# Kernel optimization log

Measured on AMD Instinct MI355X. Metric: run time of the kernel, lower is better.

The kernel has to match this reference:

```python
import jax, jax.numpy as jnp
import numpy as np

N_OBJ, N_REL = 5000, 20000
HID, POOL, N_RELCLS, N_OBJCLS = 512, 4096, 51, 151


def setup_inputs() -> dict:
    key = jax.random.key(0)
    ks = jax.random.split(key, 8)
    s = lambda fi, fo: (2.0 / (fi + fo)) ** 0.5  # xavier-ish scale
    return {
        'edge_ctx': jax.random.normal(ks[0], (N_OBJ, HID), jnp.float32),
        'union_features': jax.random.normal(ks[1], (N_REL, POOL), jnp.float32),
        'W_pe': jax.random.normal(ks[2], (2 * HID, HID), jnp.float32) * (10.0 * (1.0 / HID) ** 0.5),
        'b_pe': jnp.zeros((2 * HID,), jnp.float32),
        'W_pc': jax.random.normal(ks[3], (POOL, 2 * HID), jnp.float32) * s(2 * HID, POOL),
        'b_pc': jnp.zeros((POOL,), jnp.float32),
        'W_cc': jax.random.normal(ks[4], (N_RELCLS, POOL), jnp.float32) * s(POOL, N_RELCLS),
        'b_cc': jnp.zeros((N_RELCLS,), jnp.float32),
        'freq_emb': jax.random.normal(ks[5], (N_OBJCLS * N_OBJCLS, N_RELCLS), jnp.float32) * 0.1,
        'obj_preds': jax.random.randint(ks[6], (N_OBJ,), 0, N_OBJCLS, jnp.int64 if jax.config.jax_enable_x64 else jnp.int32),
        'pair_idx': jax.random.randint(ks[7], (N_REL, 2), 0, N_OBJ, jnp.int64 if jax.config.jax_enable_x64 else jnp.int32),
    }


def reference(edge_ctx, union_features, W_pe, b_pe, W_pc, b_pc, W_cc, b_cc,
              freq_emb, obj_preds, pair_idx):
    # post_emb -> relu -> split into head/tail halves ([N,2,HID] view)
    edge_rep = jax.nn.relu(edge_ctx @ W_pe.T + b_pe)          # [N, 2*HID]
    head_rep, tail_rep = edge_rep[:, :HID], edge_rep[:, HID:]

    hi, ti = pair_idx[:, 0], pair_idx[:, 1]
    prod = jnp.concatenate([head_rep[hi], tail_rep[ti]], axis=-1)  # [R, 2*HID]
    prod_rep = prod @ W_pc.T + b_pc                               # [R, POOL]

    ctx_dists = (prod_rep * union_features) @ W_cc.T + b_cc      # [R, 51]

    # frequency bias: embedding lookup at head_cls * num_obj_cls + tail_cls
    pair_lbl = obj_preds[hi] * N_OBJCLS + obj_preds[ti]
    frq_dists = freq_emb[pair_lbl]                               # [R, 51]
    # dropout p=0.3 is identity in eval mode
    return ctx_dists + frq_dists
```

## Files before the change

### kernel.cpp

```cpp
#include <hip/hip_runtime.h>

typedef unsigned short u16;
typedef unsigned int u32;
typedef __attribute__((ext_vector_type(4))) float f32x4;
typedef __attribute__((ext_vector_type(8))) __bf16 bf16x8;
typedef __attribute__((ext_vector_type(8))) u16 u16x8;

__device__ __forceinline__ u16 f2bf(float x) {
  u32 u = __float_as_uint(x);
  u32 r = (u + 0x7FFFu + ((u >> 16) & 1u)) >> 16;
  return (u16)r;
}

__device__ __forceinline__ float bf2f(u16 b) {
  return __uint_as_float((u32)b << 16);
}

__device__ __forceinline__ void gl16(const void* g, void* l) {
  auto* gp = (__attribute__((address_space(1))) u32*)(g);
  auto* lp = (__attribute__((address_space(3))) u32*)(l);
  __builtin_amdgcn_global_load_lds(gp, lp, 16, 0, 0);
}

__device__ __forceinline__ f32x4 mfma16(bf16x8 a, bf16x8 b, f32x4 c) {
  return __builtin_amdgcn_mfma_f32_16x16x32_bf16(a, b, c, 0, 0, 0);
}

__device__ __forceinline__ u16x8 cvt8(const float* p) {
  float4 a = *(const float4*)p, b = *(const float4*)(p + 4);
  u16x8 v;
  v[0] = f2bf(a.x); v[1] = f2bf(a.y); v[2] = f2bf(a.z); v[3] = f2bf(a.w);
  v[4] = f2bf(b.x); v[5] = f2bf(b.y); v[6] = f2bf(b.z); v[7] = f2bf(b.w);
  return v;
}

__global__ void k_prep(const float* __restrict__ ec, const float* __restrict__ wpe,
                       const float* __restrict__ wpc, const float* __restrict__ wcc,
                       u16* __restrict__ ecb, u16* __restrict__ wpeb,
                       u16* __restrict__ wpcb, u16* __restrict__ wccb) {
  int i = blockIdx.x * 256 + threadIdx.x;
  if (i < 320000) {
    *(u16x8*)(ecb + (long)i * 8) = cvt8(ec + (long)i * 8);
  } else if (i < 385536) {
    int j = i - 320000;
    *(u16x8*)(wpeb + (long)j * 8) = cvt8(wpe + (long)j * 8);
  } else if (i < 909824) {
    int j = i - 385536;
    *(u16x8*)(wpcb + (long)j * 8) = cvt8(wpc + (long)j * 8);
  } else if (i < 942592) {
    int j = i - 909824;
    long base = (long)j * 8;
    int row = (int)(base >> 12);
    int col = (int)(base & 4095);
    u16x8 v;
    if (row < 51) {
      v = cvt8(wcc + (long)row * 4096 + col);
    } else {
#pragma unroll
      for (int k = 0; k < 8; ++k) v[k] = 0;
    }
    *(u16x8*)(wccb + base) = v;
  }
}

__device__ __forceinline__ void cstep(const char* sA, const char* sB,
                                      const int (&aOff)[4], const int (&bOff)[4],
                                      f32x4 (&acc)[4][4]) {
  bf16x8 af[4], bv[4];
#pragma unroll
  for (int mi = 0; mi < 4; ++mi) af[mi] = *(const bf16x8*)(sA + aOff[mi]);
#pragma unroll
  for (int ni = 0; ni < 4; ++ni) bv[ni] = *(const bf16x8*)(sB + bOff[ni]);
  __builtin_amdgcn_s_setprio(1);
#pragma unroll
  for (int mi = 0; mi < 4; ++mi)
#pragma unroll
    for (int ni = 0; ni < 4; ++ni)
      acc[mi][ni] = mfma16(af[mi], bv[ni], acc[mi][ni]);
  __builtin_amdgcn_s_setprio(0);
}

__global__ __launch_bounds__(256, 2) void k_gemm1(const u16* __restrict__ A, const u16* __restrict__ B,
                                                  const float* __restrict__ bias, u16* __restrict__ outp) {
  __shared__ char lds[65536];
  int bx = blockIdx.x;
  int rb = bx >> 3, nb = bx & 7;
  int rowBase = rb * 128, nBase = nb * 128;
  int t = threadIdx.x, lane = t & 63, wid = t >> 6;
  int wr = wid >> 1, wc = wid & 1, lm = lane & 15, lg = lane >> 4;
  int ar0 = t >> 2, ar1 = 64 + ar0, c4 = t & 3;
  int sw0 = (c4 * 16) ^ (((ar0 >> 1) & 3) << 4);
  int sw1 = (c4 * 16) ^ (((ar1 >> 1) & 3) << 4);
  const char* aS0 = (const char*)(A + (long)min(rowBase + ar0, 4999) * 512) + sw0;
  const char* aS1 = (const char*)(A + (long)min(rowBase + ar1, 4999) * 512) + sw1;
  const char* bS0 = (const char*)(B + (long)(nBase + ar0) * 512) + sw0;
  const char* bS1 = (const char*)(B + (long)(nBase + ar1) * 512) + sw1;
  int t16 = t * 16;
  int aOff[4], bOff[4];
#pragma unroll
  for (int mi = 0; mi < 4; ++mi) { int r = wr * 64 + mi * 16 + lm; aOff[mi] = r * 64 + ((lg * 16) ^ (((r >> 1) & 3) << 4)); }
#pragma unroll
  for (int ni = 0; ni < 4; ++ni) { int r = wc * 64 + ni * 16 + lm; bOff[ni] = r * 64 + ((lg * 16) ^ (((r >> 1) & 3) << 4)); }
  f32x4 acc[4][4] = {};

#define STAGE_G(k, sb) do { \
    gl16(aS0 + (k) * 2, (sb) + t16); gl16(aS1 + (k) * 2, (sb) + 4096 + t16); \
    gl16(bS0 + (k) * 2, (sb) + 8192 + t16); gl16(bS1 + (k) * 2, (sb) + 12288 + t16); \
  } while (0)

  STAGE_G(0, lds);
  STAGE_G(32, lds + 16384);
  STAGE_G(64, lds + 32768);

  int cur = 0, stg = 3;
  for (int kt = 0; kt < 16; ++kt) {
    if (kt < 13) {
      char* sb = lds + stg * 16384;
      STAGE_G((kt + 3) * 32, sb);
    }
    if (kt < 13)       asm volatile("s_waitcnt vmcnt(12)" ::: "memory");
    else if (kt == 13) asm volatile("s_waitcnt vmcnt(8)" ::: "memory");
    else if (kt == 14) asm volatile("s_waitcnt vmcnt(4)" ::: "memory");
    else               asm volatile("s_waitcnt vmcnt(0)" ::: "memory");
    __builtin_amdgcn_s_barrier();
    char* cb = lds + cur * 16384;
    cstep(cb, cb + 8192, aOff, bOff, acc);
    __builtin_amdgcn_s_barrier();
    cur = (cur == 3) ? 0 : cur + 1;
    stg = (stg == 3) ? 0 : stg + 1;
  }
#undef STAGE_G

#pragma unroll
  for (int mi = 0; mi < 4; ++mi)
#pragma unroll
    for (int ni = 0; ni < 4; ++ni) {
      int n = nBase + wc * 64 + ni * 16 + lm;
      float bvv = bias[n];
#pragma unroll
      for (int rg = 0; rg < 4; ++rg) {
        int r = rowBase + wr * 64 + mi * 16 + lg * 4 + rg;
        if (r < 5000) {
          float v = acc[mi][ni][rg] + bvv;
          v = v > 0.f ? v : 0.f;
          outp[(long)r * 1024 + n] = f2bf(v);
        }
      }
    }
}

__global__ __launch_bounds__(256, 2) void k_gemm2(const u16* __restrict__ erep, const u16* __restrict__ wpc,
                                                  const float* __restrict__ bpc, u16* __restrict__ Hout,
                                                  u16* __restrict__ Tout) {
  __shared__ char lds[65536];
  int bx = blockIdx.x;
  int h = (bx >= 1280) ? 1 : 0;
  int rr = bx - h * 1280;
  int rb = rr >> 5, nb = rr & 31;
  int rowBase = rb * 128, nBase = nb * 128;
  u16* outp = h ? Tout : Hout;
  int t = threadIdx.x, lane = t & 63, wid = t >> 6;
  int wr = wid >> 1, wc = wid & 1, lm = lane & 15, lg = lane >> 4;
  int ar0 = t >> 2, ar1 = 64 + ar0, c4 = t & 3;
  int sw0 = (c4 * 16) ^ (((ar0 >> 1) & 3) << 4);
  int sw1 = (c4 * 16) ^ (((ar1 >> 1) & 3) << 4);
  const char* aS0 = (const char*)(erep + (long)min(rowBase + ar0, 4999) * 1024 + h * 512) + sw0;
  const char* aS1 = (const char*)(erep + (long)min(rowBase + ar1, 4999) * 1024 + h * 512) + sw1;
  const char* bS0 = (const char*)(wpc + (long)(nBase + ar0) * 1024 + h * 512) + sw0;
  const char* bS1 = (const char*)(wpc + (long)(nBase + ar1) * 1024 + h * 512) + sw1;
  int t16 = t * 16;
  int aOff[4], bOff[4];
#pragma unroll
  for (int mi = 0; mi < 4; ++mi) { int r = wr * 64 + mi * 16 + lm; aOff[mi] = r * 64 + ((lg * 16) ^ (((r >> 1) & 3) << 4)); }
#pragma unroll
  for (int ni = 0; ni < 4; ++ni) { int r = wc * 64 + ni * 16 + lm; bOff[ni] = r * 64 + ((lg * 16) ^ (((r >> 1) & 3) << 4)); }
  f32x4 acc[4][4] = {};

#define STAGE_G2(k, sb) do { \
    gl16(aS0 + (k) * 2, (sb) + t16); gl16(aS1 + (k) * 2, (sb) + 4096 + t16); \
    gl16(bS0 + (k) * 2, (sb) + 8192 + t16); gl16(bS1 + (k) * 2, (sb) + 12288 + t16); \
  } while (0)

  STAGE_G2(0, lds);
  STAGE_G2(32, lds + 16384);
  STAGE_G2(64, lds + 32768);

  int cur = 0, stg = 3;
  for (int kt = 0; kt < 16; ++kt) {
    if (kt < 13) {
      char* sb = lds + stg * 16384;
      STAGE_G2((kt + 3) * 32, sb);
    }
    if (kt < 13)       asm volatile("s_waitcnt vmcnt(12)" ::: "memory");
    else if (kt == 13) asm volatile("s_waitcnt vmcnt(8)" ::: "memory");
    else if (kt == 14) asm volatile("s_waitcnt vmcnt(4)" ::: "memory");
    else               asm volatile("s_waitcnt vmcnt(0)" ::: "memory");
    __builtin_amdgcn_s_barrier();
    char* cb = lds + cur * 16384;
    cstep(cb, cb + 8192, aOff, bOff, acc);
    __builtin_amdgcn_s_barrier();
    cur = (cur == 3) ? 0 : cur + 1;
    stg = (stg == 3) ? 0 : stg + 1;
  }
#undef STAGE_G2

#pragma unroll
  for (int mi = 0; mi < 4; ++mi)
#pragma unroll
    for (int ni = 0; ni < 4; ++ni) {
      int n = nBase + wc * 64 + ni * 16 + lm;
      float bvv = h ? 0.f : bpc[n];
#pragma unroll
      for (int rg = 0; rg < 4; ++rg) {
        int r = rowBase + wr * 64 + mi * 16 + lg * 4 + rg;
        if (r < 5000) {
          float v = acc[mi][ni][rg] + bvv;
          outp[(long)r * 4096 + n] = f2bf(v);
        }
      }
    }
}

__global__ __launch_bounds__(256) void k_final(
    const u16* __restrict__ H, const u16* __restrict__ T,
    const u16* __restrict__ wcc,
    const float* __restrict__ un,
    const int* __restrict__ pidx,
    float* __restrict__ partial) {
  __shared__ char sU[2][16384];
  int bx = blockIdx.x;
  int rb = bx >> 3, ps = bx & 7;
  int rowBase = rb * 64;
  int t = threadIdx.x, lane = t & 63, wid = t >> 6;
  int lm = lane & 15, lg = lane >> 4;
  int r16 = t >> 4, c16 = t & 15;

  u32 hoff[4], toff[4], uoff[4];
#pragma unroll
  for (int p = 0; p < 4; ++p) {
    int rG = min(rowBase + p * 16 + r16, 19999);
    hoff[p] = (u32)pidx[2 * rG] * 8192u + (u32)c16 * 16u;
    toff[p] = (u32)pidx[2 * rG + 1] * 8192u + (u32)c16 * 16u;
    uoff[p] = (u32)rG * 16384u + (u32)c16 * 32u;
  }
  const char* Hc = (const char*)H;
  const char* Tc = (const char*)T;
  const char* Uc = (const char*)un;
  int pc0 = ps * 512;

  u16x8 h8[4], t8[4];
  float4 u0[4], u1[4];

#define ISSUE(pcB) do { \
    _Pragma("unroll") \
    for (int p = 0; p < 4; ++p) { \
      h8[p] = *(const u16x8*)(Hc + hoff[p] + (u32)(pcB) * 2u); \
      t8[p] = *(const u16x8*)(Tc + toff[p] + (u32)(pcB) * 2u); \
      u0[p] = *(const float4*)(Uc + uoff[p] + (u32)(pcB) * 4u); \
      u1[p] = *(const float4*)(Uc + uoff[p] + (u32)(pcB) * 4u + 16u); \
    } \
  } while (0)

  f32x4 outAcc[4] = {};

  ISSUE(pc0);

  for (int chk = 0; chk < 4; ++chk) {
    int pcBase = pc0 + chk * 128;
    asm volatile("s_waitcnt vmcnt(0)" ::: "memory");
    char* sUb = sU[chk & 1];
#pragma unroll
    for (int p = 0; p < 4; ++p) {
      int r = p * 16 + r16;
      float uu[8];
      *(float4*)(uu) = u0[p];
      *(float4*)(uu + 4) = u1[p];
      bf16x8 pv;
#pragma unroll
      for (int j = 0; j < 8; ++j)
        pv[j] = (__bf16)((bf2f(h8[p][j]) + bf2f(t8[p][j])) * uu[j]);
      *(bf16x8*)(sUb + r * 256 + ((c16 * 16) ^ ((r & 7) << 4))) = pv;
    }
    bf16x8 bW[4][4];
#pragma unroll
    for (int kb = 0; kb < 4; ++kb)
#pragma unroll
      for (int ni = 0; ni < 4; ++ni)
        bW[kb][ni] = *(const bf16x8*)(wcc + (long)(ni * 16 + lm) * 4096 + pcBase + kb * 32 + lg * 8);
    if (chk < 3) ISSUE(pcBase + 128);
    asm volatile("s_waitcnt lgkmcnt(0)" ::: "memory");
    __builtin_amdgcn_s_barrier();

#pragma unroll
    for (int kb = 0; kb < 4; ++kb) {
      int r = wid * 16 + lm;
      bf16x8 aU = *(const bf16x8*)(sUb + r * 256 + ((kb * 64 + lg * 16) ^ ((r & 7) << 4)));
      __builtin_amdgcn_s_setprio(1);
#pragma unroll
      for (int ni = 0; ni < 4; ++ni)
        outAcc[ni] = mfma16(aU, bW[kb][ni], outAcc[ni]);
      __builtin_amdgcn_s_setprio(0);
    }
  }
#undef ISSUE

#pragma unroll
  for (int rg = 0; rg < 4; ++rg) {
    int r = wid * 16 + lg * 4 + rg;
    int rG = rowBase + r;
    if (rG < 20000) {
      long base = ((long)ps * 20000 + rG) * 64;
#pragma unroll
      for (int ni = 0; ni < 4; ++ni) {
        int c = ni * 16 + lm;
        if (c < 51) partial[base + c] = outAcc[ni][rg];
      }
    }
  }
}

__global__ void k_red(const float* __restrict__ partial, const float* __restrict__ bcc,
                      const float* __restrict__ freq, const int* __restrict__ preds,
                      const int* __restrict__ pidx, float* __restrict__ outp) {
  int idx = blockIdx.x * 256 + threadIdx.x;
  if (idx >= 20000 * 64) return;
  int row = idx >> 6, c = idx & 63;
  if (c >= 51) return;
  float s = 0.f;
#pragma unroll
  for (int i = 0; i < 8; ++i) s += partial[((long)i * 20000 + row) * 64 + c];
  int lbl = preds[pidx[2 * row]] * 151 + preds[pidx[2 * row + 1]];
  outp[(long)row * 51 + c] = s + bcc[c] + freq[(long)lbl * 51 + c];
}

extern "C" void kernel_launch(void* const* d_in, const int* in_sizes, int n_in,
                              void* d_out, int out_size, void* d_ws, size_t ws_size,
                              hipStream_t stream) {
  const float* edge_ctx = (const float*)d_in[0];
  const float* unionf   = (const float*)d_in[1];
  const float* W_pe     = (const float*)d_in[2];
  const float* b_pe     = (const float*)d_in[3];
  const float* W_pc     = (const float*)d_in[4];
  const float* b_pc     = (const float*)d_in[5];
  const float* W_cc     = (const float*)d_in[6];
  const float* b_cc     = (const float*)d_in[7];
  const float* freq     = (const float*)d_in[8];
  const int*   preds    = (const int*)d_in[9];
  const int*   pidx     = (const int*)d_in[10];
  float* out = (float*)d_out;
  char* ws = (char*)d_ws;

  u16* Hb    = (u16*)(ws + 0);
  u16* Tb    = (u16*)(ws + 40960000);
  u16* erep  = (u16*)(ws + 81920000);
  u16* wpcb  = (u16*)(ws + 92160000);
  u16* wccb  = (u16*)(ws + 100548608);
  u16* ecb   = (u16*)(ws + 101072896);
  u16* wpeb  = (u16*)(ws + 106192896);
  float* par = (float*)(ws + 107241472);

  k_prep<<<3682, 256, 0, stream>>>(edge_ctx, W_pe, W_pc, W_cc, ecb, wpeb, wpcb, wccb);
  k_gemm1<<<320, 256, 0, stream>>>(ecb, wpeb, b_pe, erep);
  k_gemm2<<<2560, 256, 0, stream>>>(erep, wpcb, b_pc, Hb, Tb);
  k_final<<<2504, 256, 0, stream>>>(Hb, Tb, wccb, unionf, pidx, par);
  k_red<<<5000, 256, 0, stream>>>(par, b_cc, freq, preds, pidx, out);
}
```

Before: 263.4 us.

## Split fused gather-multiply-GEMV into elementwise kernel plus pipelined GEMM

The fused final kernel, which gathered head/tail rows, multiplied them by union features and ran the MFMA reduction against W_cc, becomes two kernels. A grid-stride elementwise kernel writes the bf16 product matrix to workspace. A new GEMM then streams that product and W_cc through a four-stage LDS pipeline using direct global-to-LDS loads, with 128-row tiles and an 8-way K split. This aims to separate the latency-bound gather from the MFMA loop so each can be scheduled well, but it adds an extra round trip of a roughly 160 MB intermediate through memory.

```diff
diff --git a/kernel.cpp b/kernel.cpp
--- a/kernel.cpp
+++ b/kernel.cpp
@@ -221,102 +221,108 @@
     }
 }
 
-__global__ __launch_bounds__(256) void k_final(
-    const u16* __restrict__ H, const u16* __restrict__ T,
-    const u16* __restrict__ wcc,
-    const float* __restrict__ un,
-    const int* __restrict__ pidx,
-    float* __restrict__ partial) {
-  __shared__ char sU[2][16384];
+__global__ void k_mul(const u16* __restrict__ H, const u16* __restrict__ T,
+                      const float* __restrict__ un, const int* __restrict__ pidx,
+                      u16* __restrict__ P) {
+  long stride = (long)gridDim.x * 256;
+  for (long g = (long)blockIdx.x * 256 + threadIdx.x; g < 10240000; g += stride) {
+    int row = (int)(g >> 9);
+    int c8 = ((int)g & 511) * 8;
+    int hi = pidx[2 * row], ti = pidx[2 * row + 1];
+    u16x8 h8 = *(const u16x8*)(H + (long)hi * 4096 + c8);
+    u16x8 t8 = *(const u16x8*)(T + (long)ti * 4096 + c8);
+    const float* up = un + (long)row * 4096 + c8;
+    float4 u0 = *(const float4*)up, u1 = *(const float4*)(up + 4);
+    float uu[8];
+    *(float4*)(uu) = u0;
+    *(float4*)(uu + 4) = u1;
+    bf16x8 pv;
+#pragma unroll
+    for (int j = 0; j < 8; ++j)
+      pv[j] = (__bf16)((bf2f(h8[j]) + bf2f(t8[j])) * uu[j]);
+    *(bf16x8*)(P + g * 8) = pv;
+  }
+}
+
+__global__ __launch_bounds__(256, 2) void k_gemm3(const u16* __restrict__ P, const u16* __restrict__ wcc,
+                                                  float* __restrict__ partial) {
+  __shared__ char lds[49152];
   int bx = blockIdx.x;
-  int rb = bx >> 3, ps = bx & 7;
-  int rowBase = rb * 64;
+  int rb = bx >> 3, ks = bx & 7;
+  int rowBase = rb * 128;
+  long ksB = (long)ks * 1024;
   int t = threadIdx.x, lane = t & 63, wid = t >> 6;
   int lm = lane & 15, lg = lane >> 4;
-  int r16 = t >> 4, c16 = t & 15;
-
-  u32 hoff[4], toff[4], uoff[4];
-#pragma unroll
-  for (int p = 0; p < 4; ++p) {
-    int rG = min(rowBase + p * 16 + r16, 19999);
-    hoff[p] = (u32)pidx[2 * rG] * 8192u + (u32)c16 * 16u;
-    toff[p] = (u32)pidx[2 * rG + 1] * 8192u + (u32)c16 * 16u;
-    uoff[p] = (u32)rG * 16384u + (u32)c16 * 32u;
-  }
-  const char* Hc = (const char*)H;
-  const char* Tc = (const char*)T;
-  const char* Uc = (const char*)un;
-  int pc0 = ps * 512;
-
-  u16x8 h8[4], t8[4];
-  float4 u0[4], u1[4];
-
-#define ISSUE(pcB) do { \
-    _Pragma("unroll") \
-    for (int p = 0; p < 4; ++p) { \
-      h8[p] = *(const u16x8*)(Hc + hoff[p] + (u32)(pcB) * 2u); \
-      t8[p] = *(const u16x8*)(Tc + toff[p] + (u32)(pcB) * 2u); \
-      u0[p] = *(const float4*)(Uc + uoff[p] + (u32)(pcB) * 4u); \
-      u1[p] = *(const float4*)(Uc + uoff[p] + (u32)(pcB) * 4u + 16u); \
-    } \
+  int ar0 = t >> 2, ar1 = 64 + ar0, c4 = t & 3;
+  int sw0 = (c4 * 16) ^ (((ar0 >> 1) & 3) << 4);
+  int sw1 = (c4 * 16) ^ (((ar1 >> 1) & 3) << 4);
+  const char* aS0 = (const char*)P + (long)min(rowBase + ar0, 19999) * 8192 + ksB + sw0;
+  const char* aS1 = (const char*)P + (long)min(rowBase + ar1, 19999) * 8192 + ksB + sw1;
+  const char* wS  = (const char*)wcc + (long)ar0 * 8192 + ksB + sw0;
+  int t16 = t * 16;
+  int aOff[2], bOff[4];
+#pragma unroll
+  for (int m2 = 0; m2 < 2; ++m2) { int r = wid * 32 + m2 * 16 + lm; aOff[m2] = r * 64 + ((lg * 16) ^ (((r >> 1) & 3) << 4)); }
+#pragma unroll
+  for (int ni = 0; ni < 4; ++ni) { int c = ni * 16 + lm; bOff[ni] = 8192 + c * 64 + ((lg * 16) ^ (((c >> 1) & 3) << 4)); }
+  f32x4 acc[2][4] = {};
+
+#define STAGE_G3(k, sb) do { \
+    gl16(aS0 + (k) * 2, (sb) + t16); gl16(aS1 + (k) * 2, (sb) + 4096 + t16); \
+    gl16(wS + (k) * 2, (sb) + 8192 + t16); \
   } while (0)
 
-  f32x4 outAcc[4] = {};
-
-  ISSUE(pc0);
-
-  for (int chk = 0; chk < 4; ++chk) {
-    int pcBase = pc0 + chk * 128;
-    asm volatile("s_waitcnt vmcnt(0)" ::: "memory");
-    char* sUb = sU[chk & 1];
-#pragma unroll
-    for (int p = 0; p < 4; ++p) {
-      int r = p * 16 + r16;
-      float uu[8];
-      *(float4*)(uu) = u0[p];
-      *(float4*)(uu + 4) = u1[p];
-      bf16x8 pv;
-#pragma unroll
-      for (int j = 0; j < 8; ++j)
-        pv[j] = (__bf16)((bf2f(h8[p][j]) + bf2f(t8[p][j])) * uu[j]);
-      *(bf16x8*)(sUb + r * 256 + ((c16 * 16) ^ ((r & 7) << 4))) = pv;
-    }
-    bf16x8 bW[4][4];
-#pragma unroll
-    for (int kb = 0; kb < 4; ++kb)
-#pragma unroll
-      for (int ni = 0; ni < 4; ++ni)
-        bW[kb][ni] = *(const bf16x8*)(wcc + (long)(ni * 16 + lm) * 4096 + pcBase + kb * 32 + lg * 8);
-    if (chk < 3) ISSUE(pcBase + 128);
-    asm volatile("s_waitcnt lgkmcnt(0)" ::: "memory");
-    __builtin_amdgcn_s_barrier();
-
-#pragma unroll
-    for (int kb = 0; kb < 4; ++kb) {
-      int r = wid * 16 + lm;
-      bf16x8 aU = *(const bf16x8*)(sUb + r * 256 + ((kb * 64 + lg * 16) ^ ((r & 7) << 4)));
+  STAGE_G3(0, lds);
+  STAGE_G3(32, lds + 12288);
+  STAGE_G3(64, lds + 24576);
+
+  int cur = 0, stg = 3;
+  for (int kt = 0; kt < 16; ++kt) {
+    if (kt < 13) {
+      char* sb = lds + stg * 12288;
+      STAGE_G3((kt + 3) * 32, sb);
+    }
+    if (kt < 13)       asm volatile("s_waitcnt vmcnt(9)" ::: "memory");
+    else if (kt == 13) asm volatile("s_waitcnt vmcnt(6)" ::: "memory");
+    else if (kt == 14) asm volatile("s_waitcnt vmcnt(3)" ::: "memory");
+    else               asm volatile("s_waitcnt vmcnt(0)" ::: "memory");
+    __builtin_amdgcn_s_barrier();
+    char* cb = lds + cur * 12288;
+    {
+      bf16x8 aU[2], bW[4];
+#pragma unroll
+      for (int m2 = 0; m2 < 2; ++m2) aU[m2] = *(const bf16x8*)(cb + aOff[m2]);
+#pragma unroll
+      for (int ni = 0; ni < 4; ++ni) bW[ni] = *(const bf16x8*)(cb + bOff[ni]);
       __builtin_amdgcn_s_setprio(1);
 #pragma unroll
-      for (int ni = 0; ni < 4; ++ni)
-        outAcc[ni] = mfma16(aU, bW[kb][ni], outAcc[ni]);
+      for (int m2 = 0; m2 < 2; ++m2)
+#pragma unroll
+        for (int ni = 0; ni < 4; ++ni)
+          acc[m2][ni] = mfma16(aU[m2], bW[ni], acc[m2][ni]);
       __builtin_amdgcn_s_setprio(0);
     }
-  }
-#undef ISSUE
-
-#pragma unroll
-  for (int rg = 0; rg < 4; ++rg) {
-    int r = wid * 16 + lg * 4 + rg;
-    int rG = rowBase + r;
-    if (rG < 20000) {
-      long base = ((long)ps * 20000 + rG) * 64;
-#pragma unroll
-      for (int ni = 0; ni < 4; ++ni) {
-        int c = ni * 16 + lm;
-        if (c < 51) partial[base + c] = outAcc[ni][rg];
+    __builtin_amdgcn_s_barrier();
+    cur = (cur == 3) ? 0 : cur + 1;
+    stg = (stg == 3) ? 0 : stg + 1;
+  }
+#undef STAGE_G3
+
+#pragma unroll
+  for (int m2 = 0; m2 < 2; ++m2)
+#pragma unroll
+    for (int rg = 0; rg < 4; ++rg) {
+      int r = wid * 32 + m2 * 16 + lg * 4 + rg;
+      int rG = rowBase + r;
+      if (rG < 20000) {
+        long base = ((long)ks * 20000 + rG) * 64;
+#pragma unroll
+        for (int ni = 0; ni < 4; ++ni) {
+          int c = ni * 16 + lm;
+          if (c < 51) partial[base + c] = acc[m2][ni][rg];
+        }
       }
     }
-  }
 }
 
 __global__ void k_red(const float* __restrict__ partial, const float* __restrict__ bcc,
@@ -358,10 +364,12 @@
   u16* ecb   = (u16*)(ws + 101072896);
   u16* wpeb  = (u16*)(ws + 106192896);
   float* par = (float*)(ws + 107241472);
+  u16* Pb    = (u16*)(ws + 148201472);
 
   k_prep<<<3682, 256, 0, stream>>>(edge_ctx, W_pe, W_pc, W_cc, ecb, wpeb, wpcb, wccb);
   k_gemm1<<<320, 256, 0, stream>>>(ecb, wpeb, b_pe, erep);
   k_gemm2<<<2560, 256, 0, stream>>>(erep, wpcb, b_pc, Hb, Tb);
-  k_final<<<2504, 256, 0, stream>>>(Hb, Tb, wccb, unionf, pidx, par);
+  k_mul<<<2048, 256, 0, stream>>>(Hb, Tb, unionf, pidx, Pb);
+  k_gemm3<<<1256, 256, 0, stream>>>(Pb, wccb, par);
   k_red<<<5000, 256, 0, stream>>>(par, b_cc, freq, preds, pidx, out);
 }
```

Measured after the change: 296.0 us. +12.4%, slower.
